# Kernel optimization log

Hardware: AMD Instinct MI355X
Metric: run time of the kernel (lower is better)

The kernel has to match this reference:

```python
import jax, jax.numpy as jnp
import numpy as np

# Mamba2 dims (from source: d_model=2048, d_state=64, d_conv=4, expand=2; defaults headdim=64, ngroups=1)
D_MODEL = 2048
D_STATE = 64
D_CONV = 4
EXPAND = 2
HEADDIM = 64
D_INNER = EXPAND * D_MODEL            # 4096
NHEADS = D_INNER // HEADDIM           # 64
NGROUPS = 1
CONV_DIM = D_INNER + 2 * NGROUPS * D_STATE   # 4224
D_IN_PROJ = 2 * D_INNER + 2 * NGROUPS * D_STATE + NHEADS  # 8384
N_CLASSES = 4
EPS = 1e-5


def setup_inputs() -> dict:
    key = jax.random.key(0)
    ks = jax.random.split(key, 10)
    b, l = 4, 2048
    x = jax.random.normal(ks[0], (b, l, D_MODEL), dtype=jnp.float32)
    in_proj_w = jax.random.normal(ks[1], (D_IN_PROJ, D_MODEL), dtype=jnp.float32) * 0.02
    conv_w = jax.random.normal(ks[2], (CONV_DIM, D_CONV), dtype=jnp.float32) * 0.2
    conv_b = jnp.zeros((CONV_DIM,), dtype=jnp.float32)
    # dt_bias s.t. softplus(dt_bias) in [0.001, 0.1]
    dt = jax.random.uniform(ks[3], (NHEADS,), minval=0.001, maxval=0.1)
    dt_bias = jnp.log(jnp.expm1(dt)).astype(jnp.float32)
    # A in [1, 16] per head
    A_log = jnp.log(jax.random.uniform(ks[4], (NHEADS,), minval=1.0, maxval=16.0)).astype(jnp.float32)
    D = jnp.ones((NHEADS,), dtype=jnp.float32)
    norm_w = jnp.ones((D_INNER,), dtype=jnp.float32)
    out_proj_w = jax.random.normal(ks[5], (D_MODEL, D_INNER), dtype=jnp.float32) * 0.02
    cls_w = jax.random.normal(ks[6], (N_CLASSES, D_MODEL), dtype=jnp.float32) * 0.02
    cls_b = jnp.zeros((N_CLASSES,), dtype=jnp.float32)
    return {"x": x, "in_proj_w": in_proj_w, "conv_w": conv_w, "conv_b": conv_b,
            "dt_bias": dt_bias, "A_log": A_log, "D": D, "norm_w": norm_w,
            "out_proj_w": out_proj_w, "cls_w": cls_w, "cls_b": cls_b}


def _mamba2_forward(x, in_proj_w, conv_w, conv_b, dt_bias, A_log, D, norm_w, out_proj_w):
    b, l, _ = x.shape
    zxbcdt = jnp.einsum('bld,ed->ble', x, in_proj_w)  # (b,l,8384)
    z = zxbcdt[..., :D_INNER]
    xBC = zxbcdt[..., D_INNER:D_INNER + CONV_DIM]
    dt_raw = zxbcdt[..., D_INNER + CONV_DIM:]         # (b,l,nheads)

    # causal depthwise conv1d (kernel D_CONV), then SiLU
    xp = jnp.pad(xBC, ((0, 0), (D_CONV - 1, 0), (0, 0)))
    conv_out = conv_b
    for k in range(D_CONV):
        conv_out = conv_out + xp[:, k:k + l, :] * conv_w[:, k]
    xBC = jax.nn.silu(conv_out)

    xh = xBC[..., :D_INNER].reshape(b, l, NHEADS, HEADDIM)
    Bm = xBC[..., D_INNER:D_INNER + D_STATE]          # (b,l,n) ngroups=1
    Cm = xBC[..., D_INNER + D_STATE:]                 # (b,l,n)

    dt = jax.nn.softplus(dt_raw + dt_bias)           # (b,l,h)
    dA = jnp.exp(dt * (-jnp.exp(A_log)))             # (b,l,h)
    dtx = dt[..., None] * xh                          # (b,l,h,p)

    xs = (dA.transpose(1, 0, 2), dtx.transpose(1, 0, 2, 3),
          Bm.transpose(1, 0, 2), Cm.transpose(1, 0, 2))

    def step(hst, inp):
        dA_t, dtx_t, B_t, C_t = inp
        # hst: (b,h,p,n)
        hst = hst * dA_t[:, :, None, None] + dtx_t[..., None] * B_t[:, None, None, :]
        y_t = jnp.einsum('bhpn,bn->bhp', hst, C_t)
        return hst, y_t

    h0 = jnp.zeros((b, NHEADS, HEADDIM, D_STATE), dtype=x.dtype)
    _, ys = jax.lax.scan(step, h0, xs)               # (l,b,h,p)
    y = ys.transpose(1, 0, 2, 3) + D[None, None, :, None] * xh
    y = y.reshape(b, l, D_INNER)

    # RMSNormGated (norm_before_gate=False): rmsnorm(y * silu(z)) * weight
    y = y * jax.nn.silu(z)
    y = y * jax.lax.rsqrt(jnp.mean(y * y, axis=-1, keepdims=True) + EPS) * norm_w
    return jnp.einsum('ble,de->bld', y, out_proj_w)   # (b,l,d_model)


def reference(x, in_proj_w, conv_w, conv_b, dt_bias, A_log, D, norm_w, out_proj_w, cls_w, cls_b):
    h = _mamba2_forward(x, in_proj_w, conv_w, conv_b, dt_bias, A_log, D, norm_w, out_proj_w)
    return jnp.einsum('bld,cd->blc', h, cls_w) + cls_b  # (b,l,4)
```

## Files before the change

kernel.cpp:

```cpp
#include <hip/hip_runtime.h>

#define BB 4
#define LL 2048
#define DMODEL 2048
#define DSTATE 64
#define DCONV 4
#define DINNER 4096
#define NHEADS 64
#define CONVDIM 4224
#define DINPROJ 8384
#define NPAD1   8448
#define MROWS 8192
#define DTROW0 8320

typedef short bf16x8 __attribute__((ext_vector_type(8)));
typedef float f32x4  __attribute__((ext_vector_type(4)));
typedef __attribute__((address_space(1))) void as1_void;
typedef __attribute__((address_space(3))) void as3_void;

__device__ inline unsigned short f2bf(float f) {
  unsigned int u = __float_as_uint(f);
  u += 0x7FFF + ((u >> 16) & 1);
  return (unsigned short)(u >> 16);
}
__device__ inline float bf2f(unsigned short u) {
  return __uint_as_float(((unsigned int)u) << 16);
}

__global__ void f32_to_bf16_kernel(const float* __restrict__ in,
                                   unsigned short* __restrict__ out, long nquads) {
  long q = (long)blockIdx.x * 256 + threadIdx.x;
  if (q >= nquads) return;
  float4 v = ((const float4*)in)[q];
  ushort4 o;
  o.x = f2bf(v.x); o.y = f2bf(v.y); o.z = f2bf(v.z); o.w = f2bf(v.w);
  ((ushort4*)out)[q] = o;
}

__global__ void convert_w1_kernel(const float* __restrict__ w,
                                  unsigned short* __restrict__ out) {
  long q = (long)blockIdx.x * 256 + threadIdx.x;
  long row = q >> 9;
  ushort4 o; o.x = 0; o.y = 0; o.z = 0; o.w = 0;
  if (row < DINPROJ) {
    float4 v = ((const float4*)w)[q];
    o.x = f2bf(v.x); o.y = f2bf(v.y); o.z = f2bf(v.z); o.w = f2bf(v.w);
  }
  ((ushort4*)out)[q] = o;
}

template <bool BF16OUT>
__global__ __launch_bounds__(256) void gemm_mfma(
    const unsigned short* __restrict__ A,
    const unsigned short* __restrict__ B,
    void* __restrict__ Cv, int M, int N, int K) {
  __shared__ __align__(16) char sA[128 * 128];
  __shared__ __align__(16) char sB[128 * 128];
  const int tid  = threadIdx.x;
  const int lane = tid & 63;
  const int wave = tid >> 6;
  const long m0 = (long)blockIdx.y * 128;
  const long n0 = (long)blockIdx.x * 128;
  const int wm = (wave >> 1) * 64;
  const int wn = (wave & 1) * 64;
  const int fr = lane & 15;
  const int kb = lane >> 4;
  const int xr = (fr & 7) << 4;
  const size_t strideA = (size_t)K * 2;

  f32x4 acc[4][4] = {};

  for (int k0 = 0; k0 < K; k0 += 64) {
    __syncthreads();
#pragma unroll
    for (int u = 0; u < 4; ++u) {
      const int idx  = u * 256 + tid;
      const int row  = idx >> 3;
      const int csrc = ((idx & 7) << 4) ^ ((row & 7) << 4);
      const char* ga = (const char*)A + (size_t)(m0 + row) * strideA + (size_t)k0 * 2 + csrc;
      const char* gb = (const char*)B + (size_t)(n0 + row) * strideA + (size_t)k0 * 2 + csrc;
      __builtin_amdgcn_global_load_lds((as1_void*)ga, (as3_void*)(sA + idx * 16), 16, 0, 0);
      __builtin_amdgcn_global_load_lds((as1_void*)gb, (as3_void*)(sB + idx * 16), 16, 0, 0);
    }
    __syncthreads();
#pragma unroll
    for (int kh = 0; kh < 2; ++kh) {
      bf16x8 af[4], bg[4];
      const int cread = (kh * 64 + kb * 16) ^ xr;
#pragma unroll
      for (int i = 0; i < 4; ++i) {
        const int ar = wm + i * 16 + fr;
        af[i] = *(const bf16x8*)(sA + ar * 128 + cread);
        const int br = wn + i * 16 + fr;
        bg[i] = *(const bf16x8*)(sB + br * 128 + cread);
      }
#pragma unroll
      for (int i = 0; i < 4; ++i)
#pragma unroll
        for (int j = 0; j < 4; ++j)
          acc[i][j] = __builtin_amdgcn_mfma_f32_16x16x32_bf16(af[i], bg[j], acc[i][j], 0, 0, 0);
    }
  }

#pragma unroll
  for (int i = 0; i < 4; ++i) {
    const long mbase = m0 + wm + i * 16 + kb * 4;
#pragma unroll
    for (int j = 0; j < 4; ++j) {
      const long n = n0 + wn + j * 16 + fr;
      if (n < N) {
#pragma unroll
        for (int r = 0; r < 4; ++r) {
          const long m = mbase + r;
          if (BF16OUT) ((unsigned short*)Cv)[m * (long)N + n] = f2bf(acc[i][j][r]);
          else         ((float*)Cv)[m * (long)N + n] = acc[i][j][r];
        }
      }
    }
  }
}

__global__ void dt_kernel(const float* __restrict__ x,
                          const float* __restrict__ w,
                          const float* __restrict__ dt_bias,
                          const float* __restrict__ A_log,
                          float* __restrict__ dtv, float* __restrict__ dAv) {
  __shared__ float s_w[64][129];
  __shared__ float s_x[16][129];
  const int tid = threadIdx.x;
  const int row0 = blockIdx.x * 16;
  const int c = tid & 63;
  const int rg = tid >> 6;
  float acc[4] = {0.f, 0.f, 0.f, 0.f};
  for (int k0 = 0; k0 < DMODEL; k0 += 128) {
    __syncthreads();
#pragma unroll
    for (int u = 0; u < 32; ++u) {
      int idx = u * 256 + tid;
      int r = idx >> 7, kk = idx & 127;
      s_w[r][kk] = w[(size_t)(DTROW0 + r) * DMODEL + k0 + kk];
    }
#pragma unroll
    for (int u = 0; u < 8; ++u) {
      int idx = u * 256 + tid;
      int r = idx >> 7, kk = idx & 127;
      s_x[r][kk] = x[(size_t)(row0 + r) * DMODEL + k0 + kk];
    }
    __syncthreads();
    for (int kk = 0; kk < 128; ++kk) {
      float wv = s_w[c][kk];
#pragma unroll
      for (int j = 0; j < 4; ++j) acc[j] += s_x[rg * 4 + j][kk] * wv;
    }
  }
  const float a = expf(A_log[c]);
  const float bias = dt_bias[c];
#pragma unroll
  for (int j = 0; j < 4; ++j) {
    int row = row0 + rg * 4 + j;
    float v = acc[j] + bias;
    float dt = (v > 20.f) ? v : log1pf(expf(v));
    dtv[(size_t)row * 64 + c] = dt;
    dAv[(size_t)row * 64 + c] = expf(-dt * a);
  }
}

__global__ void conv_kernel(const unsigned short* __restrict__ zxb,
                            const float* __restrict__ conv_w,
                            const float* __restrict__ conv_b,
                            unsigned short* __restrict__ xh,
                            float* __restrict__ Bm,
                            float* __restrict__ Cm) {
  const int row = blockIdx.x;
  const int l = row & (LL - 1);
  for (int c = threadIdx.x; c < CONVDIM; c += 256) {
    float acc = conv_b[c];
#pragma unroll
    for (int k = 0; k < DCONV; ++k) {
      int ll = l - (DCONV - 1) + k;
      if (ll >= 0) {
        size_t rr = (size_t)row + (ll - l);
        acc += bf2f(zxb[rr * DINPROJ + DINNER + c]) * conv_w[c * DCONV + k];
      }
    }
    float s = acc / (1.f + expf(-acc));
    if (c < DINNER)               xh[(size_t)row * DINNER + c] = f2bf(s);
    else if (c < DINNER + DSTATE) Bm[(size_t)row * DSTATE + (c - DINNER)] = s;
    else                          Cm[(size_t)row * DSTATE + (c - DINNER - DSTATE)] = s;
  }
}

#define CT 16
__global__ void scan_kernel(const unsigned short* xh,
                            const float* __restrict__ Bm,
                            const float* __restrict__ Cm,
                            const float* __restrict__ dtv,
                            const float* __restrict__ dAv,
                            const float* __restrict__ Dv,
                            unsigned short* y) {
  __shared__ __align__(16) float s_x[CT][64];
  __shared__ __align__(16) float s_B[CT][64];
  __shared__ __align__(16) float s_C[CT][64];
  __shared__ __align__(16) float s_y[CT][64];
  __shared__ float s_dt[CT], s_dA[CT];
  const int b = blockIdx.x >> 6;
  const int head = blockIdx.x & 63;
  const int tid = threadIdx.x;
  const int p = tid >> 2, q = tid & 3, n0 = q * 16;
  const float Dh = Dv[head];
  float h[16];
#pragma unroll
  for (int i = 0; i < 16; ++i) h[i] = 0.f;

  for (int t0 = 0; t0 < LL; t0 += CT) {
    __syncthreads();
#pragma unroll
    for (int u = 0; u < CT * 64 / 256; ++u) {
      int idx = u * 256 + tid;
      int tt = idx >> 6, cc = idx & 63;
      size_t r = (size_t)(b * LL + t0 + tt);
      s_x[tt][cc] = bf2f(xh[r * DINNER + head * 64 + cc]);
      s_B[tt][cc] = Bm[r * 64 + cc];
      s_C[tt][cc] = Cm[r * 64 + cc];
    }
    if (tid < CT) {
      size_t r = (size_t)(b * LL + t0 + tid);
      s_dt[tid] = dtv[r * 64 + head];
      s_dA[tid] = dAv[r * 64 + head];
    }
    __syncthreads();
    for (int tt = 0; tt < CT; ++tt) {
      float dA = s_dA[tt], dt = s_dt[tt];
      float xp = s_x[tt][p];
      float dtx = dt * xp;
      const float4* Bp = (const float4*)&s_B[tt][n0];
      const float4* Cp = (const float4*)&s_C[tt][n0];
      float ys = 0.f;
#pragma unroll
      for (int i = 0; i < 4; ++i) {
        float4 bv = Bp[i];
        float4 cv = Cp[i];
        h[4*i+0] = h[4*i+0] * dA + dtx * bv.x;  ys += h[4*i+0] * cv.x;
        h[4*i+1] = h[4*i+1] * dA + dtx * bv.y;  ys += h[4*i+1] * cv.y;
        h[4*i+2] = h[4*i+2] * dA + dtx * bv.z;  ys += h[4*i+2] * cv.z;
        h[4*i+3] = h[4*i+3] * dA + dtx * bv.w;  ys += h[4*i+3] * cv.w;
      }
      ys += __shfl_xor(ys, 1);
      ys += __shfl_xor(ys, 2);
      if (q == 0) s_y[tt][p] = ys + Dh * xp;
    }
    __syncthreads();
#pragma unroll
    for (int u = 0; u < CT * 64 / 256; ++u) {
      int idx = u * 256 + tid;
      int tt = idx >> 6, cc = idx & 63;
      size_t r = (size_t)(b * LL + t0 + tt);
      y[r * DINNER + head * 64 + cc] = f2bf(s_y[tt][cc]);
    }
  }
}

__global__ void norm_kernel(const unsigned short* y,
                            const unsigned short* __restrict__ zxb,
                            const float* __restrict__ norm_w,
                            unsigned short* ynb) {
  const int row = blockIdx.x;
  const int tid = threadIdx.x;
  float g[16];
  float ss = 0.f;
#pragma unroll
  for (int i = 0; i < 16; ++i) {
    int d = i * 256 + tid;
    float zv = bf2f(zxb[(size_t)row * DINPROJ + d]);
    float gv = bf2f(y[(size_t)row * DINNER + d]) * (zv / (1.f + expf(-zv)));
    g[i] = gv;
    ss += gv * gv;
  }
#pragma unroll
  for (int off = 32; off >= 1; off >>= 1) ss += __shfl_xor(ss, off);
  __shared__ float sred[4];
  __shared__ float s_rs;
  if ((tid & 63) == 0) sred[tid >> 6] = ss;
  __syncthreads();
  if (tid == 0) {
    float tot = sred[0] + sred[1] + sred[2] + sred[3];
    s_rs = rsqrtf(tot / (float)DINNER + 1e-5f);
  }
  __syncthreads();
  float rs = s_rs;
#pragma unroll
  for (int i = 0; i < 16; ++i) {
    int d = i * 256 + tid;
    ynb[(size_t)row * DINNER + d] = f2bf(g[i] * rs * norm_w[d]);
  }
}

__global__ void cls_kernel(const float* __restrict__ h,
                           const float* __restrict__ cls_w,
                           const float* __restrict__ cls_b,
                           float* __restrict__ out) {
  const int row = blockIdx.x;
  const int tid = threadIdx.x;
  float a0 = 0, a1 = 0, a2 = 0, a3 = 0;
  for (int d = tid; d < DMODEL; d += 256) {
    float hv = h[(size_t)row * DMODEL + d];
    a0 += hv * cls_w[d];
    a1 += hv * cls_w[DMODEL + d];
    a2 += hv * cls_w[2 * DMODEL + d];
    a3 += hv * cls_w[3 * DMODEL + d];
  }
#pragma unroll
  for (int off = 32; off >= 1; off >>= 1) {
    a0 += __shfl_xor(a0, off); a1 += __shfl_xor(a1, off);
    a2 += __shfl_xor(a2, off); a3 += __shfl_xor(a3, off);
  }
  __shared__ float sred[4][4];
  if ((tid & 63) == 0) { int w = tid >> 6; sred[w][0] = a0; sred[w][1] = a1; sred[w][2] = a2; sred[w][3] = a3; }
  __syncthreads();
  if (tid < 4) {
    float s = sred[0][tid] + sred[1][tid] + sred[2][tid] + sred[3][tid] + cls_b[tid];
    out[(size_t)row * 4 + tid] = s;
  }
}

extern "C" void kernel_launch(void* const* d_in, const int* in_sizes, int n_in,
                              void* d_out, int out_size, void* d_ws, size_t ws_size,
                              hipStream_t stream) {
  const float* x          = (const float*)d_in[0];
  const float* in_proj_w  = (const float*)d_in[1];
  const float* conv_w     = (const float*)d_in[2];
  const float* conv_b     = (const float*)d_in[3];
  const float* dt_bias    = (const float*)d_in[4];
  const float* A_log      = (const float*)d_in[5];
  const float* Dv         = (const float*)d_in[6];
  const float* norm_w     = (const float*)d_in[7];
  const float* out_proj_w = (const float*)d_in[8];
  const float* cls_w      = (const float*)d_in[9];
  const float* cls_b      = (const float*)d_in[10];

  char* ws = (char*)d_ws;
  unsigned short* zxb = (unsigned short*)(ws + 0);
  unsigned short* xh  = (unsigned short*)(ws + 137363456);
  float*          Bmp = (float*)(ws + 204472320);
  float*          Cmp = (float*)(ws + 206569472);
  float*          dtv = (float*)(ws + 208666624);
  float*          dAv = (float*)(ws + 210763776);
  unsigned short* ynb  = xh;
  float*          hbuf = (float*)zxb;
  unsigned short* xbf = xh;
  unsigned short* w1b = (unsigned short*)((char*)xh + 33554432);
  unsigned short* w2b = (unsigned short*)((char*)zxb + 67108864);

  f32_to_bf16_kernel<<<16384, 256, 0, stream>>>(x, xbf, 4194304);
  convert_w1_kernel<<<16896, 256, 0, stream>>>(in_proj_w, w1b);

  dt_kernel<<<512, 256, 0, stream>>>(x, in_proj_w, dt_bias, A_log, dtv, dAv);

  gemm_mfma<true><<<dim3(NPAD1 / 128, MROWS / 128), 256, 0, stream>>>(
      xbf, w1b, zxb, MROWS, DINPROJ, DMODEL);

  conv_kernel<<<MROWS, 256, 0, stream>>>(zxb, conv_w, conv_b, xh, Bmp, Cmp);

  scan_kernel<<<256, 256, 0, stream>>>(xh, Bmp, Cmp, dtv, dAv, Dv, xh);

  norm_kernel<<<MROWS, 256, 0, stream>>>(xh, zxb, norm_w, ynb);

  f32_to_bf16_kernel<<<8192, 256, 0, stream>>>(out_proj_w, w2b, 2097152);

  gemm_mfma<false><<<dim3(DMODEL / 128, MROWS / 128), 256, 0, stream>>>(
      ynb, w2b, hbuf, MROWS, DMODEL, DINNER);

  cls_kernel<<<MROWS, 256, 0, stream>>>(hbuf, cls_w, cls_b, (float*)d_out);
}
```

Measured before the change: 1.663 ms.

## Parallelize selective scan across chunks with state propagation; split in_proj output

The sequential scan, which ran only 256 blocks each walking all 2048 timesteps, is replaced by a three-phase chunked scan. The phases are per-chunk end states with decay products, a sequential propagation across 16 chunks, and a per-chunk apply seeded with the carried-in state. This gives 16x more blocks to use the GPU's compute units. The in_proj GEMM now writes z and xBC to separate compact buffers, so the conv and norm kernels read with tighter strides. The cost is extra passes over x, B and dt plus intermediate state buffers in the workspace.

```diff
diff --git a/kernel.cpp b/kernel.cpp
--- a/kernel.cpp
+++ b/kernel.cpp
@@ -12,6 +12,7 @@
 #define NPAD1   8448
 #define MROWS 8192
 #define DTROW0 8320
+#define XBCCOLS 4288
 
 typedef short bf16x8 __attribute__((ext_vector_type(8)));
 typedef float f32x4  __attribute__((ext_vector_type(4)));
@@ -49,11 +50,12 @@
   ((ushort4*)out)[q] = o;
 }
 
-template <bool BF16OUT>
+template <bool BF16OUT, bool SPLIT>
 __global__ __launch_bounds__(256) void gemm_mfma(
     const unsigned short* __restrict__ A,
     const unsigned short* __restrict__ B,
-    void* __restrict__ Cv, int M, int N, int K) {
+    void* __restrict__ Cv, void* __restrict__ Cv2,
+    int M, int N, int K, int Nsplit, int ld2) {
   __shared__ __align__(16) char sA[128 * 128];
   __shared__ __align__(16) char sB[128 * 128];
   const int tid  = threadIdx.x;
@@ -112,8 +114,14 @@
 #pragma unroll
         for (int r = 0; r < 4; ++r) {
           const long m = mbase + r;
-          if (BF16OUT) ((unsigned short*)Cv)[m * (long)N + n] = f2bf(acc[i][j][r]);
-          else         ((float*)Cv)[m * (long)N + n] = acc[i][j][r];
+          if (!SPLIT || n < Nsplit) {
+            const long ld = SPLIT ? Nsplit : N;
+            if (BF16OUT) ((unsigned short*)Cv)[m * ld + n] = f2bf(acc[i][j][r]);
+            else         ((float*)Cv)[m * ld + n] = acc[i][j][r];
+          } else {
+            if (BF16OUT) ((unsigned short*)Cv2)[m * (long)ld2 + (n - Nsplit)] = f2bf(acc[i][j][r]);
+            else         ((float*)Cv2)[m * (long)ld2 + (n - Nsplit)] = acc[i][j][r];
+          }
         }
       }
     }
@@ -165,7 +173,7 @@
   }
 }
 
-__global__ void conv_kernel(const unsigned short* __restrict__ zxb,
+__global__ void conv_kernel(const unsigned short* __restrict__ xbc,
                             const float* __restrict__ conv_w,
                             const float* __restrict__ conv_b,
                             unsigned short* __restrict__ xh,
@@ -180,7 +188,7 @@
       int ll = l - (DCONV - 1) + k;
       if (ll >= 0) {
         size_t rr = (size_t)row + (ll - l);
-        acc += bf2f(zxb[rr * DINPROJ + DINNER + c]) * conv_w[c * DCONV + k];
+        acc += bf2f(xbc[rr * XBCCOLS + c]) * conv_w[c * DCONV + k];
       }
     }
     float s = acc / (1.f + expf(-acc));
@@ -191,40 +199,141 @@
 }
 
 #define CT 16
-__global__ void scan_kernel(const unsigned short* xh,
-                            const float* __restrict__ Bm,
-                            const float* __restrict__ Cm,
-                            const float* __restrict__ dtv,
-                            const float* __restrict__ dAv,
-                            const float* __restrict__ Dv,
-                            unsigned short* y) {
+#define CHUNK 128
+#define NCHUNK 16
+
+__global__ void scan_state_kernel(const unsigned short* __restrict__ xhp,
+                                  const float* __restrict__ Bm,
+                                  const float* __restrict__ dtv,
+                                  const float* __restrict__ dAv,
+                                  float* __restrict__ hend,
+                                  float* __restrict__ chunkA) {
+  __shared__ __align__(16) float s_x[CT][64];
+  __shared__ __align__(16) float s_B[CT][64];
+  __shared__ float s_dt[CT], s_dA[CT];
+  const int chunk = blockIdx.x & (NCHUNK - 1);
+  const int bh = blockIdx.x >> 4;
+  const int head = bh & 63;
+  const int b = bh >> 6;
+  const int tid = threadIdx.x;
+  const int p = tid >> 2, q = tid & 3, n0 = q * 16;
+  float h[16];
+#pragma unroll
+  for (int i = 0; i < 16; ++i) h[i] = 0.f;
+  float pA = 1.f;
+  const int tbase = b * LL + chunk * CHUNK;
+
+  for (int t0 = 0; t0 < CHUNK; t0 += CT) {
+    __syncthreads();
+#pragma unroll
+    for (int u = 0; u < CT * 64 / 256; ++u) {
+      int idx = u * 256 + tid;
+      int tt = idx >> 6, cc = idx & 63;
+      size_t r = (size_t)(tbase + t0 + tt);
+      s_x[tt][cc] = bf2f(xhp[r * DINNER + head * 64 + cc]);
+      s_B[tt][cc] = Bm[r * 64 + cc];
+    }
+    if (tid < CT) {
+      size_t r = (size_t)(tbase + t0 + tid);
+      s_dt[tid] = dtv[r * 64 + head];
+      s_dA[tid] = dAv[r * 64 + head];
+    }
+    __syncthreads();
+    for (int tt = 0; tt < CT; ++tt) {
+      float dA = s_dA[tt];
+      float dtx = s_dt[tt] * s_x[tt][p];
+      pA *= dA;
+      const float4* Bp = (const float4*)&s_B[tt][n0];
+#pragma unroll
+      for (int i = 0; i < 4; ++i) {
+        float4 bv = Bp[i];
+        h[4*i+0] = h[4*i+0] * dA + dtx * bv.x;
+        h[4*i+1] = h[4*i+1] * dA + dtx * bv.y;
+        h[4*i+2] = h[4*i+2] * dA + dtx * bv.z;
+        h[4*i+3] = h[4*i+3] * dA + dtx * bv.w;
+      }
+    }
+  }
+  float* hp = hend + ((size_t)bh * NCHUNK + chunk) * 4096 + tid * 16;
+#pragma unroll
+  for (int i = 0; i < 4; ++i) {
+    float4 v; v.x = h[4*i]; v.y = h[4*i+1]; v.z = h[4*i+2]; v.w = h[4*i+3];
+    ((float4*)hp)[i] = v;
+  }
+  if (tid == 0) chunkA[bh * NCHUNK + chunk] = pA;
+}
+
+__global__ void scan_prop_kernel(float* __restrict__ hend,
+                                 const float* __restrict__ chunkA) {
+  const int bh = blockIdx.x;
+  const int tid = threadIdx.x;
+  float cr[16];
+#pragma unroll
+  for (int i = 0; i < 16; ++i) cr[i] = 0.f;
+  for (int c = 0; c < NCHUNK; ++c) {
+    float* hp = hend + ((size_t)bh * NCHUNK + c) * 4096 + tid * 16;
+    const float a = chunkA[bh * NCHUNK + c];
+    float e[16];
+#pragma unroll
+    for (int i = 0; i < 4; ++i) {
+      float4 v = ((float4*)hp)[i];
+      e[4*i] = v.x; e[4*i+1] = v.y; e[4*i+2] = v.z; e[4*i+3] = v.w;
+    }
+#pragma unroll
+    for (int i = 0; i < 4; ++i) {
+      float4 v; v.x = cr[4*i]; v.y = cr[4*i+1]; v.z = cr[4*i+2]; v.w = cr[4*i+3];
+      ((float4*)hp)[i] = v;
+    }
+#pragma unroll
+    for (int i = 0; i < 16; ++i) cr[i] = cr[i] * a + e[i];
+  }
+}
+
+__global__ void scan_apply_kernel(const unsigned short* xhp,
+                                  const float* __restrict__ Bm,
+                                  const float* __restrict__ Cm,
+                                  const float* __restrict__ dtv,
+                                  const float* __restrict__ dAv,
+                                  const float* __restrict__ Dv,
+                                  const float* __restrict__ hstart,
+                                  unsigned short* y) {
   __shared__ __align__(16) float s_x[CT][64];
   __shared__ __align__(16) float s_B[CT][64];
   __shared__ __align__(16) float s_C[CT][64];
   __shared__ __align__(16) float s_y[CT][64];
   __shared__ float s_dt[CT], s_dA[CT];
-  const int b = blockIdx.x >> 6;
-  const int head = blockIdx.x & 63;
+  const int chunk = blockIdx.x & (NCHUNK - 1);
+  const int bh = blockIdx.x >> 4;
+  const int head = bh & 63;
+  const int b = bh >> 6;
   const int tid = threadIdx.x;
   const int p = tid >> 2, q = tid & 3, n0 = q * 16;
   const float Dh = Dv[head];
+  const int tbase = b * LL + chunk * CHUNK;
+
   float h[16];
-#pragma unroll
-  for (int i = 0; i < 16; ++i) h[i] = 0.f;
-
-  for (int t0 = 0; t0 < LL; t0 += CT) {
+  {
+    const float* hp = hstart + ((size_t)bh * NCHUNK + chunk) * 4096 + tid * 16;
+#pragma unroll
+    for (int i = 0; i < 4; ++i) {
+      float4 v = ((const float4*)hp)[i];
+      h[4*i] = v.x; h[4*i+1] = v.y; h[4*i+2] = v.z; h[4*i+3] = v.w;
+    }
+  }
+
+  for (int t0 = 0; t0 < CHUNK; t0 += CT) {
     __syncthreads();
 #pragma unroll
     for (int u = 0; u < CT * 64 / 256; ++u) {
       int idx = u * 256 + tid;
       int tt = idx >> 6, cc = idx & 63;
-      size_t r = (size_t)(b * LL + t0 + tt);
-      s_x[tt][cc] = bf2f(xh[r * DINNER + head * 64 + cc]);
+      size_t r = (size_t)(tbase + t0 + tt);
+      s_x[tt][cc] = bf2f(xhp[r * DINNER + head * 64 + cc]);
       s_B[tt][cc] = Bm[r * 64 + cc];
       s_C[tt][cc] = Cm[r * 64 + cc];
     }
     if (tid < CT) {
-      size_t r = (size_t)(b * LL + t0 + tid);
+      size_t r = (size_t)(tbase + t0 + tid);
       s_dt[tid] = dtv[r * 64 + head];
       s_dA[tid] = dAv[r * 64 + head];
     }
@@ -254,14 +363,14 @@
     for (int u = 0; u < CT * 64 / 256; ++u) {
       int idx = u * 256 + tid;
       int tt = idx >> 6, cc = idx & 63;
-      size_t r = (size_t)(b * LL + t0 + tt);
+      size_t r = (size_t)(tbase + t0 + tt);
       y[r * DINNER + head * 64 + cc] = f2bf(s_y[tt][cc]);
     }
   }
 }
 
 __global__ void norm_kernel(const unsigned short* y,
-                            const unsigned short* __restrict__ zxb,
+                            const unsigned short* __restrict__ zbuf,
                             const float* __restrict__ norm_w,
                             unsigned short* ynb) {
   const int row = blockIdx.x;
@@ -271,7 +380,7 @@
 #pragma unroll
   for (int i = 0; i < 16; ++i) {
     int d = i * 256 + tid;
-    float zv = bf2f(zxb[(size_t)row * DINPROJ + d]);
+    float zv = bf2f(zbuf[(size_t)row * DINNER + d]);
     float gv = bf2f(y[(size_t)row * DINNER + d]) * (zv / (1.f + expf(-zv)));
     g[i] = gv;
     ss += gv * gv;
@@ -339,36 +448,41 @@
   const float* cls_b      = (const float*)d_in[10];
 
   char* ws = (char*)d_ws;
-  unsigned short* zxb = (unsigned short*)(ws + 0);
-  unsigned short* xh  = (unsigned short*)(ws + 137363456);
-  float*          Bmp = (float*)(ws + 204472320);
-  float*          Cmp = (float*)(ws + 206569472);
-  float*          dtv = (float*)(ws + 208666624);
-  float*          dAv = (float*)(ws + 210763776);
+  unsigned short* zbuf = (unsigned short*)(ws + 0);
+  unsigned short* xbc  = (unsigned short*)(ws + 67108864);
+  unsigned short* xh   = (unsigned short*)(ws + 137363456);
+  float*          Bmp  = (float*)(ws + 204472320);
+  float*          Cmp  = (float*)(ws + 206569472);
+  float*          dtv  = (float*)(ws + 208666624);
+  float*          dAv  = (float*)(ws + 210763776);
   unsigned short* ynb  = xh;
-  float*          hbuf = (float*)zxb;
+  float*          hbuf = (float*)zbuf;
   unsigned short* xbf = xh;
   unsigned short* w1b = (unsigned short*)((char*)xh + 33554432);
-  unsigned short* w2b = (unsigned short*)((char*)zxb + 67108864);
+  float*          hend   = (float*)xbc;
+  float*          chunkA = (float*)((char*)xbc + 67108864);
+  unsigned short* w2b = (unsigned short*)xbc;
 
   f32_to_bf16_kernel<<<16384, 256, 0, stream>>>(x, xbf, 4194304);
   convert_w1_kernel<<<16896, 256, 0, stream>>>(in_proj_w, w1b);
 
   dt_kernel<<<512, 256, 0, stream>>>(x, in_proj_w, dt_bias, A_log, dtv, dAv);
 
-  gemm_mfma<true><<<dim3(NPAD1 / 128, MROWS / 128), 256, 0, stream>>>(
-      xbf, w1b, zxb, MROWS, DINPROJ, DMODEL);
-
-  conv_kernel<<<MROWS, 256, 0, stream>>>(zxb, conv_w, conv_b, xh, Bmp, Cmp);
-
-  scan_kernel<<<256, 256, 0, stream>>>(xh, Bmp, Cmp, dtv, dAv, Dv, xh);
-
-  norm_kernel<<<MROWS, 256, 0, stream>>>(xh, zxb, norm_w, ynb);
+  gemm_mfma<true, true><<<dim3(NPAD1 / 128, MROWS / 128), 256, 0, stream>>>(
+      xbf, w1b, zbuf, xbc, MROWS, DINPROJ, DMODEL, DINNER, XBCCOLS);
+
+  conv_kernel<<<MROWS, 256, 0, stream>>>(xbc, conv_w, conv_b, xh, Bmp, Cmp);
+
+  scan_state_kernel<<<256 * NCHUNK, 256, 0, stream>>>(xh, Bmp, dtv, dAv, hend, chunkA);
+  scan_prop_kernel<<<256, 256, 0, stream>>>(hend, chunkA);
+  scan_apply_kernel<<<256 * NCHUNK, 256, 0, stream>>>(xh, Bmp, Cmp, dtv, dAv, Dv, hend, xh);
+
+  norm_kernel<<<MROWS, 256, 0, stream>>>(xh, zbuf, norm_w, ynb);
 
   f32_to_bf16_kernel<<<8192, 256, 0, stream>>>(out_proj_w, w2b, 2097152);
 
-  gemm_mfma<false><<<dim3(DMODEL / 128, MROWS / 128), 256, 0, stream>>>(
-      ynb, w2b, hbuf, MROWS, DMODEL, DINNER);
+  gemm_mfma<false, false><<<dim3(DMODEL / 128, MROWS / 128), 256, 0, stream>>>(
+      ynb, w2b, hbuf, nullptr, MROWS, DMODEL, DINNER, DMODEL, 0);
 
   cls_kernel<<<MROWS, 256, 0, stream>>>(hbuf, cls_w, cls_b, (float*)d_out);
 }
```

Measured after the change: 1.568 ms. 1.06x faster.
